# Performance work log

Measured on AMD Instinct MI355X. Metric: run time of the kernel, lower is better.

The kernel has to match this reference:

```python
import jax, jax.numpy as jnp
import numpy as np

LATENT = 128
RNN = 512      # rnn_size
CODE = 2048    # code_size


def _lstm_cell(x, h, c, w_ih, w_hh, b_ih, b_hh):
    # PyTorch LSTM gate order: i, f, g, o
    gates = x @ w_ih + b_ih + h @ w_hh + b_hh
    i, f, g, o = jnp.split(gates, 4, axis=-1)
    c_new = jax.nn.sigmoid(f) * c + jax.nn.sigmoid(i) * jnp.tanh(g)
    h_new = jax.nn.sigmoid(o) * jnp.tanh(c_new)
    return h_new, c_new


def setup_inputs() -> dict:
    key = jax.random.key(0)
    ks = jax.random.split(key, 16)
    B = 1024
    s = 0.02
    inp = {
        "latent": jax.random.normal(ks[0], (B, LATENT), jnp.float32),
        "num_segments": 128,
        # unpack_idea: Linear(latent, code) + Tanh
        "w_unpack": jax.random.normal(ks[1], (LATENT, CODE), jnp.float32) * s,
        "b_unpack": jnp.zeros((CODE,), jnp.float32),
        # LSTM layer 1 (input CODE -> hidden RNN)
        "w_ih1": jax.random.normal(ks[2], (CODE, 4 * RNN), jnp.float32) * s,
        "w_hh1": jax.random.normal(ks[3], (RNN, 4 * RNN), jnp.float32) * s,
        "b_ih1": jnp.zeros((4 * RNN,), jnp.float32),
        "b_hh1": jnp.zeros((4 * RNN,), jnp.float32),
        # LSTM layer 2 (hidden RNN -> hidden RNN)
        "w_ih2": jax.random.normal(ks[4], (RNN, 4 * RNN), jnp.float32) * s,
        "w_hh2": jax.random.normal(ks[5], (RNN, 4 * RNN), jnp.float32) * s,
        "b_ih2": jnp.zeros((4 * RNN,), jnp.float32),
        "b_hh2": jnp.zeros((4 * RNN,), jnp.float32),
        # attention head: Linear(RNN, CODE) + Sigmoid
        "w_att": jax.random.normal(ks[6], (RNN, CODE), jnp.float32) * s,
        "b_att": jnp.zeros((CODE,), jnp.float32),
        # widths head: Linear(RNN, 1) + Sigmoid
        "w_wid": jax.random.normal(ks[7], (RNN, 1), jnp.float32) * s,
        "b_wid": jnp.zeros((1,), jnp.float32),
        # angles head: Linear(RNN, 1) + Tanh
        "w_ang": jax.random.normal(ks[8], (RNN, 1), jnp.float32) * s,
        "b_ang": jnp.zeros((1,), jnp.float32),
    }
    return inp


def reference(latent, num_segments, w_unpack, b_unpack,
              w_ih1, w_hh1, b_ih1, b_hh1,
              w_ih2, w_hh2, b_ih2, b_hh2,
              w_att, b_att, w_wid, b_wid, w_ang, b_ang):
    B = latent.shape[0]
    idea = jnp.tanh(latent @ w_unpack + b_unpack)  # [B, CODE]

    def step(carry, _):
        h1, c1, h2, c2, att = carry
        x = idea * att                               # gated input [B, CODE]
        h1, c1 = _lstm_cell(x, h1, c1, w_ih1, w_hh1, b_ih1, b_hh1)
        h2, c2 = _lstm_cell(h1, h2, c2, w_ih2, w_hh2, b_ih2, b_hh2)
        angles = jnp.tanh(h2 @ w_ang + b_ang)        # [B, 1]
        widths = jax.nn.sigmoid(h2 @ w_wid + b_wid)  # [B, 1]
        att = jax.nn.sigmoid(h2 @ w_att + b_att)     # [B, CODE]
        out = jnp.concatenate([angles, widths], axis=-1)  # [B, 2]
        return (h1, c1, h2, c2, att), out

    z = jnp.zeros((B, RNN), latent.dtype)
    init = (z, z, z, z, jnp.ones((B, CODE), latent.dtype))
    _, ys = jax.lax.scan(step, init, None, length=int(num_segments))
    return jnp.transpose(ys, (1, 0, 2))  # [B, num_segments, 2]
```

## Files before the change

### kernel.cpp

```cpp
#include <hip/hip_runtime.h>
#include <hip/hip_bf16.h>
#include <cmath>

typedef __attribute__((ext_vector_type(8))) short bf16x8;
typedef __attribute__((ext_vector_type(4))) float f32x4;
typedef unsigned int u32;

#define DEVI __device__ __forceinline__

DEVI float sigf(float x) { return 1.0f / (1.0f + __expf(-x)); }

typedef const __attribute__((address_space(1))) u32* gas_t;
typedef __attribute__((address_space(3))) u32* las_t;
DEVI void g2l16(const void* g, void* l) {
  __builtin_amdgcn_global_load_lds((gas_t)g, (las_t)l, 16, 0, 0);
}

#define BATCH 1024
#define CODE  2048
#define RNN   512
#define NG    2048
#define TSTEPS 128
#define K1K   2560
#define K2K   1024
#define K3K   512
#define NO    2176

#define BUFSZ 24576


__global__ void conv_w1(const float* __restrict__ w_ih1, const float* __restrict__ w_hh1,
                        __hip_bfloat16* __restrict__ W1T) {
  int np = blockIdx.x;
  int co = (np & 3) * RNN + (np >> 2);
  for (int k = threadIdx.x; k < K1K; k += 256) {
    float v = (k < CODE) ? w_ih1[(size_t)k * NG + co]
                         : w_hh1[(size_t)(k - CODE) * NG + co];
    W1T[(size_t)np * K1K + k] = __float2bfloat16(v);
  }
}

__global__ void conv_w2(const float* __restrict__ w_ih2, const float* __restrict__ w_hh2,
                        __hip_bfloat16* __restrict__ W2T) {
  int np = blockIdx.x;
  int co = (np & 3) * RNN + (np >> 2);
  for (int k = threadIdx.x; k < K2K; k += 256) {
    float v = (k < RNN) ? w_ih2[(size_t)k * NG + co]
                        : w_hh2[(size_t)(k - RNN) * NG + co];
    W2T[(size_t)np * K2K + k] = __float2bfloat16(v);
  }
}

__global__ void conv_wo(const float* __restrict__ w_att, const float* __restrict__ w_ang,
                        const float* __restrict__ w_wid, __hip_bfloat16* __restrict__ WoT) {
  int n = blockIdx.x;
  for (int k = threadIdx.x; k < K3K; k += 256) {
    float v = 0.f;
    if (n < CODE) v = w_att[(size_t)k * CODE + n];
    else if (n == CODE) v = w_ang[k];
    else if (n == CODE + 1) v = w_wid[k];
    WoT[(size_t)n * K3K + k] = __float2bfloat16(v);
  }
}

__global__ void conv_b(const float* b_ih1, const float* b_hh1,
                       const float* b_ih2, const float* b_hh2,
                       const float* b_att, const float* b_ang, const float* b_wid,
                       float* b1p, float* b2p, float* bo) {
  int i = blockIdx.x * 256 + threadIdx.x;
  if (i < NG) {
    int co = (i & 3) * RNN + (i >> 2);
    b1p[i] = b_ih1[co] + b_hh1[co];
    b2p[i] = b_ih2[co] + b_hh2[co];
  }
  if (i < NO) {
    float v = 0.f;
    if (i < CODE) v = b_att[i];
    else if (i == CODE) v = b_ang[0];
    else if (i == CODE + 1) v = b_wid[0];
    bo[i] = v;
  }
}

__global__ void init_zero(char* __restrict__ zb, char* __restrict__ xb) {
  int idx = blockIdx.x * 256 + threadIdx.x;
  f32x4 z = {0.f, 0.f, 0.f, 0.f};
  for (int i = idx; i < 393216; i += 262144) *(f32x4*)(zb + (size_t)i * 16) = z;
  for (int i = idx; i < 65536; i += 262144) {
    int row = i >> 6, j = i & 63;
    *(f32x4*)(xb + (size_t)row * (K1K * 2) + CODE * 2 + (size_t)j * 16) = z;
  }
}

__global__ void idea_kernel(const float* __restrict__ latent, const float* __restrict__ w,
                            const float* __restrict__ b,
                            __hip_bfloat16* __restrict__ idea_bf,
                            __hip_bfloat16* __restrict__ x_bf) {
  int idx = blockIdx.x * 256 + threadIdx.x;
  int bi = idx >> 11, j = idx & 2047;
  const float* lr = latent + bi * 128;
  float s = b[j];
#pragma unroll 8
  for (int k = 0; k < 128; ++k) s = fmaf(lr[k], w[(size_t)k * CODE + j], s);
  __hip_bfloat16 h = __float2bfloat16(tanhf(s));
  idea_bf[idx] = h;
  x_bf[(size_t)bi * K1K + j] = h;
}


#define STAGE(KO, DST)                                                        \
  _Pragma("unroll") for (int j = 0; j < 3; ++j)                               \
      g2l16(gp[j] + (KO), (DST) + ldsc[j]);

#define COMPUTE(SB)                                                           \
  __builtin_amdgcn_s_setprio(1);                                              \
  _Pragma("unroll") for (int kk = 0; kk < 2; ++kk) {                          \
    bf16x8 av[2], bv[2];                                                      \
    _Pragma("unroll") for (int fm = 0; fm < 2; ++fm)                          \
        av[fm] = *(const bf16x8*)((SB) + aoff[fm][kk]);                       \
    _Pragma("unroll") for (int fn = 0; fn < 2; ++fn)                          \
        bv[fn] = *(const bf16x8*)((SB) + boff[fn][kk]);                       \
    _Pragma("unroll") for (int fm = 0; fm < 2; ++fm)                          \
      _Pragma("unroll") for (int fn = 0; fn < 2; ++fn)                        \
        acc[fm][fn] = __builtin_amdgcn_mfma_f32_16x16x32_bf16(                \
            av[fm], bv[fn], acc[fm][fn], 0, 0, 0);                            \
  }                                                                           \
  __builtin_amdgcn_s_setprio(0);

#define WAITB(N)                                                              \
  asm volatile("s_waitcnt vmcnt(" #N ")" ::: "memory");                       \
  __builtin_amdgcn_s_barrier();                                               \
  asm volatile("" ::: "memory");

__global__ void __launch_bounds__(512, 2)
lstm_gemm(const char* __restrict__ Ab, const char* __restrict__ Bb,
          int K, int nk, const float* __restrict__ bias,
          float* __restrict__ c_state, __hip_bfloat16* __restrict__ h_out, int h_ld) {
  __shared__ char smem[3 * BUFSZ];
  const int tid = threadIdx.x;
  const int l = blockIdx.x;
  const int xcd = l & 7, bi = l >> 3;
  const int n0 = ((xcd << 1) | (bi & 1)) * 128;
  const int m0 = (bi >> 1) * 64;
  const int kb = K * 2;

  const int lane = tid & 63, wv = tid >> 6;
  const int rl = lane >> 3;
  const int cswz = ((lane & 7) * 16) ^ (rl << 4);

  const char* gp[3];
  int ldsc[3];
#pragma unroll
  for (int j = 0; j < 3; ++j) {
    int c = wv * 3 + j;
    int row = (c < 8) ? (m0 + c * 8 + rl) : (n0 + (c - 8) * 8 + rl);
    const char* base = (c < 8) ? Ab : Bb;
    gp[j] = base + (size_t)row * kb + cswz;
    ldsc[j] = c * 1024;
  }

  const int l16 = lane & 15, lg = lane >> 4;
  const int wr = wv & 1, wc = wv >> 1;
  const int xm = (l16 & 7) << 4;

  int aoff[2][2], boff[2][2];
#pragma unroll
  for (int fm = 0; fm < 2; ++fm) {
    int r = wr * 32 + fm * 16 + l16;
#pragma unroll
    for (int kk = 0; kk < 2; ++kk) aoff[fm][kk] = r * 128 + ((kk * 64 + lg * 16) ^ xm);
  }
#pragma unroll
  for (int fn = 0; fn < 2; ++fn) {
    int r = wc * 32 + fn * 16 + l16;
#pragma unroll
    for (int kk = 0; kk < 2; ++kk) boff[fn][kk] = 8192 + r * 128 + ((kk * 64 + lg * 16) ^ xm);
  }

  f32x4 z4 = {0.f, 0.f, 0.f, 0.f};
  f32x4 acc[2][2];
#pragma unroll
  for (int a = 0; a < 2; ++a)
#pragma unroll
    for (int b = 0; b < 2; ++b) acc[a][b] = z4;

  STAGE(0, smem);
  STAGE(128, smem + BUFSZ);

  for (int kt = 0; kt < nk - 1; ++kt) {
    WAITB(3);
    if (kt + 2 < nk) {
      char* nb = smem + ((kt + 2) % 3) * BUFSZ;
      STAGE((size_t)(kt + 2) * 128, nb);
    }
    const char* sb = smem + (kt % 3) * BUFSZ;
    COMPUTE(sb);
  }
  WAITB(0);
  COMPUTE(smem + ((nk - 1) % 3) * BUFSZ);

  __syncthreads();
  float* gsm = (float*)smem;
#pragma unroll
  for (int fm = 0; fm < 2; ++fm)
#pragma unroll
    for (int fn = 0; fn < 2; ++fn) {
      int col = wc * 32 + fn * 16 + l16;
#pragma unroll
      for (int j = 0; j < 4; ++j) {
        int row = wr * 32 + fm * 16 + lg * 4 + j;
        gsm[row * 128 + col] = acc[fm][fn][j];
      }
    }
  __syncthreads();
#pragma unroll
  for (int i = 0; i < 4; ++i) {
    int p = tid + i * 512;
    int unit = p & 31, row = p >> 5;
    f32x4 g = *(const f32x4*)(gsm + row * 128 + unit * 4);
    f32x4 bb = *(const f32x4*)(bias + n0 + unit * 4);
    float ig = sigf(g.x + bb.x);
    float fg = sigf(g.y + bb.y);
    float gg = tanhf(g.z + bb.z);
    float og = sigf(g.w + bb.w);
    int grow = m0 + row, gu = (n0 >> 2) + unit;
    float cold = c_state[grow * RNN + gu];
    float cn = fg * cold + ig * gg;
    c_state[grow * RNN + gu] = cn;
    h_out[(size_t)grow * h_ld + gu] = __float2bfloat16(og * tanhf(cn));
  }
}

__global__ void __launch_bounds__(512, 2)
att_head(const char* __restrict__ Ab, const char* __restrict__ Bb,
         const float* __restrict__ bo,
         const __hip_bfloat16* __restrict__ idea_bf,
         __hip_bfloat16* __restrict__ x_bf,
         __hip_bfloat16* __restrict__ h_cat,
         const __hip_bfloat16* __restrict__ h2b,
         float* __restrict__ out, int t) {
  __shared__ char smem[3 * BUFSZ];
  const int tid = threadIdx.x;
  const int m0 = blockIdx.x * 64;
  const int n0 = blockIdx.y * 128;
  const int kb = K3K * 2;

  if (blockIdx.y == 0) {
#pragma unroll
    for (int i = 0; i < 8; ++i) {
      int o = tid * 16 + i * 8192;
      int row = m0 + (o >> 10), cb = o & 1023;
      *(f32x4*)((char*)x_bf + (size_t)row * (K1K * 2) + CODE * 2 + cb) =
          *(const f32x4*)((const char*)h_cat + (size_t)row * (K2K * 2) + cb);
      *(f32x4*)((char*)h_cat + (size_t)row * (K2K * 2) + RNN * 2 + cb) =
          *(const f32x4*)((const char*)h2b + (size_t)row * (RNN * 2) + cb);
    }
  }

  const int lane = tid & 63, wv = tid >> 6;
  const int rl = lane >> 3;
  const int cswz = ((lane & 7) * 16) ^ (rl << 4);

  const char* gp[3];
  int ldsc[3];
#pragma unroll
  for (int j = 0; j < 3; ++j) {
    int c = wv * 3 + j;
    int row = (c < 8) ? (m0 + c * 8 + rl) : (n0 + (c - 8) * 8 + rl);
    const char* base = (c < 8) ? Ab : Bb;
    gp[j] = base + (size_t)row * kb + cswz;
    ldsc[j] = c * 1024;
  }

  const int l16 = lane & 15, lg = lane >> 4;
  const int wr = wv & 1, wc = wv >> 1;
  const int xm = (l16 & 7) << 4;

  int aoff[2][2], boff[2][2];
#pragma unroll
  for (int fm = 0; fm < 2; ++fm) {
    int r = wr * 32 + fm * 16 + l16;
#pragma unroll
    for (int kk = 0; kk < 2; ++kk) aoff[fm][kk] = r * 128 + ((kk * 64 + lg * 16) ^ xm);
  }
#pragma unroll
  for (int fn = 0; fn < 2; ++fn) {
    int r = wc * 32 + fn * 16 + l16;
#pragma unroll
    for (int kk = 0; kk < 2; ++kk) boff[fn][kk] = 8192 + r * 128 + ((kk * 64 + lg * 16) ^ xm);
  }

  f32x4 z4 = {0.f, 0.f, 0.f, 0.f};
  f32x4 acc[2][2];
#pragma unroll
  for (int a = 0; a < 2; ++a)
#pragma unroll
    for (int b = 0; b < 2; ++b) acc[a][b] = z4;

  const int nk = K3K / 64;
  STAGE(0, smem);
  STAGE(128, smem + BUFSZ);

  for (int kt = 0; kt < nk - 1; ++kt) {
    WAITB(3);
    if (kt + 2 < nk) {
      char* nb = smem + ((kt + 2) % 3) * BUFSZ;
      STAGE((size_t)(kt + 2) * 128, nb);
    }
    const char* sb = smem + (kt % 3) * BUFSZ;
    COMPUTE(sb);
  }
  WAITB(0);
  COMPUTE(smem + ((nk - 1) % 3) * BUFSZ);

#pragma unroll
  for (int fn = 0; fn < 2; ++fn) {
    int col = n0 + wc * 32 + fn * 16 + l16;
    float bia = bo[col];
    bool is_att = col < CODE;
#pragma unroll
    for (int fm = 0; fm < 2; ++fm)
#pragma unroll
      for (int j = 0; j < 4; ++j) {
        int row = m0 + wr * 32 + fm * 16 + lg * 4 + j;
        float v = acc[fm][fn][j] + bia;
        if (is_att) {
          float a = sigf(v);
          float id = __bfloat162float(idea_bf[(size_t)row * CODE + col]);
          x_bf[(size_t)row * K1K + col] = __float2bfloat16(id * a);
        } else if (col == CODE) {
          out[row * (TSTEPS * 2) + t * 2] = tanhf(v);
        } else if (col == CODE + 1) {
          out[row * (TSTEPS * 2) + t * 2 + 1] = sigf(v);
        }
      }
  }
}

extern "C" void kernel_launch(void* const* d_in, const int* in_sizes, int n_in,
                              void* d_out, int out_size, void* d_ws, size_t ws_size,
                              hipStream_t stream) {
  const float* latent = (const float*)d_in[0];
  const float* w_unp  = (const float*)d_in[2];
  const float* b_unp  = (const float*)d_in[3];
  const float* w_ih1  = (const float*)d_in[4];
  const float* w_hh1  = (const float*)d_in[5];
  const float* b_ih1  = (const float*)d_in[6];
  const float* b_hh1  = (const float*)d_in[7];
  const float* w_ih2  = (const float*)d_in[8];
  const float* w_hh2  = (const float*)d_in[9];
  const float* b_ih2  = (const float*)d_in[10];
  const float* b_hh2  = (const float*)d_in[11];
  const float* w_att  = (const float*)d_in[12];
  const float* b_att  = (const float*)d_in[13];
  const float* w_wid  = (const float*)d_in[14];
  const float* b_wid  = (const float*)d_in[15];
  const float* w_ang  = (const float*)d_in[16];
  const float* b_ang  = (const float*)d_in[17];
  float* out = (float*)d_out;

  char* ws = (char*)d_ws;
  __hip_bfloat16* W1T  = (__hip_bfloat16*)(ws + 0);
  __hip_bfloat16* W2T  = (__hip_bfloat16*)(ws + 10485760);
  __hip_bfloat16* WoT  = (__hip_bfloat16*)(ws + 14680064);
  float* b1p           = (float*)(ws + 16908288);
  float* b2p           = (float*)(ws + 16916480);
  float* bo            = (float*)(ws + 16924672);
  __hip_bfloat16* idea = (__hip_bfloat16*)(ws + 16933376);
  __hip_bfloat16* x_bf = (__hip_bfloat16*)(ws + 21127680);
  __hip_bfloat16* hcat = (__hip_bfloat16*)(ws + 26370560);
  float* c1            = (float*)(ws + 28467712);
  float* c2            = (float*)(ws + 30564864);
  __hip_bfloat16* h2b  = (__hip_bfloat16*)(ws + 32662016);

  conv_w1<<<2048, 256, 0, stream>>>(w_ih1, w_hh1, W1T);
  conv_w2<<<2048, 256, 0, stream>>>(w_ih2, w_hh2, W2T);
  conv_wo<<<2176, 256, 0, stream>>>(w_att, w_ang, w_wid, WoT);
  conv_b<<<9, 256, 0, stream>>>(b_ih1, b_hh1, b_ih2, b_hh2, b_att, b_ang, b_wid, b1p, b2p, bo);
  init_zero<<<1024, 256, 0, stream>>>(ws + 26370560, (char*)x_bf);
  idea_kernel<<<8192, 256, 0, stream>>>(latent, w_unp, b_unp, idea, x_bf);

  for (int t = 0; t < TSTEPS; ++t) {
    lstm_gemm<<<256, 512, 0, stream>>>((const char*)x_bf, (const char*)W1T,
                                       K1K, K1K / 64, b1p, c1, hcat, 1024);
    lstm_gemm<<<256, 512, 0, stream>>>((const char*)hcat, (const char*)W2T,
                                       K2K, K2K / 64, b2p, c2, h2b, 512);
    att_head<<<dim3(16, 17), 512, 0, stream>>>((const char*)h2b, (const char*)WoT,
                                               bo, idea, x_bf, hcat, h2b, out, t);
  }
}
```

Measured before the change: 5.710 ms.

## Split K across wave halves with 128-wide K tiles and LDS reduction

The GEMM kernels now stage 128-wide K tiles (doubled LDS buffers) and split the eight waves into two K-halves. Each wave computes a 32x64 sub-tile over half of each K tile. The two halves are then summed through padded shared memory before the LSTM and attention epilogues. The goal is fewer pipeline iterations and barriers, and more MFMA work per LDS load. In exchange it uses more LDS (144KB per block), which may lower occupancy below two blocks per CU, and it adds a reduction pass.

```diff
diff --git a/kernel.cpp b/kernel.cpp
--- a/kernel.cpp
+++ b/kernel.cpp
@@ -26,7 +26,7 @@
 #define K3K   512
 #define NO    2176
 
-#define BUFSZ 24576
+#define BUFSZ 49152
 
 
 __global__ void conv_w1(const float* __restrict__ w_ih1, const float* __restrict__ w_hh1,
@@ -109,19 +109,19 @@
 
 
 #define STAGE(KO, DST)                                                        \
-  _Pragma("unroll") for (int j = 0; j < 3; ++j)                               \
+  _Pragma("unroll") for (int j = 0; j < 6; ++j)                               \
       g2l16(gp[j] + (KO), (DST) + ldsc[j]);
 
 #define COMPUTE(SB)                                                           \
   __builtin_amdgcn_s_setprio(1);                                              \
   _Pragma("unroll") for (int kk = 0; kk < 2; ++kk) {                          \
-    bf16x8 av[2], bv[2];                                                      \
+    bf16x8 av[2], bv[4];                                                      \
     _Pragma("unroll") for (int fm = 0; fm < 2; ++fm)                          \
         av[fm] = *(const bf16x8*)((SB) + aoff[fm][kk]);                       \
-    _Pragma("unroll") for (int fn = 0; fn < 2; ++fn)                          \
+    _Pragma("unroll") for (int fn = 0; fn < 4; ++fn)                          \
         bv[fn] = *(const bf16x8*)((SB) + boff[fn][kk]);                       \
     _Pragma("unroll") for (int fm = 0; fm < 2; ++fm)                          \
-      _Pragma("unroll") for (int fn = 0; fn < 2; ++fn)                        \
+      _Pragma("unroll") for (int fn = 0; fn < 4; ++fn)                        \
         acc[fm][fn] = __builtin_amdgcn_mfma_f32_16x16x32_bf16(                \
             av[fm], bv[fn], acc[fm][fn], 0, 0, 0);                            \
   }                                                                           \
@@ -131,6 +131,74 @@
   asm volatile("s_waitcnt vmcnt(" #N ")" ::: "memory");                       \
   __builtin_amdgcn_s_barrier();                                               \
   asm volatile("" ::: "memory");
+
+#define GEMM_SETUP(AB, BB, KBYTES)                                            \
+  const int lane = tid & 63, wv = tid >> 6;                                   \
+  const char* gp[6]; int ldsc[6];                                             \
+  {                                                                           \
+    int ccol = ((lane & 15) * 16) ^ ((lane >> 4) << 4);                       \
+    _Pragma("unroll") for (int j = 0; j < 6; ++j) {                           \
+      int c = wv * 6 + j;                                                     \
+      int row = (c < 16) ? (m0 + c * 4 + (lane >> 4))                         \
+                         : (n0 + (c - 16) * 4 + (lane >> 4));                 \
+      const char* base = (c < 16) ? (AB) : (BB);                              \
+      gp[j] = base + (size_t)row * (KBYTES) + (ccol ^ ((c & 1) << 6));        \
+      ldsc[j] = c * 1024;                                                     \
+    }                                                                         \
+  }                                                                           \
+  const int l16 = lane & 15, lg = lane >> 4;                                  \
+  const int kh = wv >> 2, q = wv & 3, wr = q & 1, wc = q >> 1;                \
+  const int xm = (l16 & 7) << 4;                                              \
+  int aoff[2][2], boff[4][2];                                                 \
+  _Pragma("unroll") for (int fm = 0; fm < 2; ++fm) {                          \
+    int r = wr * 32 + fm * 16 + l16;                                          \
+    _Pragma("unroll") for (int kk = 0; kk < 2; ++kk)                          \
+      aoff[fm][kk] = r * 256 + ((kh * 128 + kk * 64 + lg * 16) ^ xm);         \
+  }                                                                           \
+  _Pragma("unroll") for (int fn = 0; fn < 4; ++fn) {                          \
+    int r = wc * 64 + fn * 16 + l16;                                          \
+    _Pragma("unroll") for (int kk = 0; kk < 2; ++kk)                          \
+      boff[fn][kk] = 16384 + r * 256 + ((kh * 128 + kk * 64 + lg * 16) ^ xm); \
+  }                                                                           \
+  f32x4 z4 = {0.f, 0.f, 0.f, 0.f};                                            \
+  f32x4 acc[2][4];                                                            \
+  _Pragma("unroll") for (int a = 0; a < 2; ++a)                               \
+    _Pragma("unroll") for (int b = 0; b < 4; ++b) acc[a][b] = z4;
+
+#define GEMM_PIPELINE(NK)                                                     \
+  STAGE(0, smem);                                                             \
+  STAGE(256, smem + BUFSZ);                                                   \
+  for (int kt = 0; kt < (NK) - 1; ++kt) {                                     \
+    WAITB(6);                                                                 \
+    if (kt + 2 < (NK)) {                                                      \
+      char* nb = smem + ((kt + 2) % 3) * BUFSZ;                               \
+      STAGE((size_t)(kt + 2) * 256, nb);                                      \
+    }                                                                         \
+    const char* sb = smem + (kt % 3) * BUFSZ;                                 \
+    COMPUTE(sb);                                                              \
+  }                                                                           \
+  WAITB(0);                                                                   \
+  COMPUTE(smem + (((NK) - 1) % 3) * BUFSZ);
+
+#define KH_COMBINE()                                                          \
+  __syncthreads();                                                            \
+  float* gsm = (float*)smem;                                                  \
+  if (kh == 1) {                                                              \
+    _Pragma("unroll") for (int fm = 0; fm < 2; ++fm)                          \
+      _Pragma("unroll") for (int fn = 0; fn < 4; ++fn)                        \
+        _Pragma("unroll") for (int j = 0; j < 4; ++j)                         \
+          gsm[(wr * 32 + fm * 16 + lg * 4 + j) * 132 +                        \
+              wc * 64 + fn * 16 + l16] = acc[fm][fn][j];                      \
+  }                                                                           \
+  __syncthreads();                                                            \
+  if (kh == 0) {                                                              \
+    _Pragma("unroll") for (int fm = 0; fm < 2; ++fm)                          \
+      _Pragma("unroll") for (int fn = 0; fn < 4; ++fn)                        \
+        _Pragma("unroll") for (int j = 0; j < 4; ++j)                         \
+          gsm[(wr * 32 + fm * 16 + lg * 4 + j) * 132 +                        \
+              wc * 64 + fn * 16 + l16] += acc[fm][fn][j];                     \
+  }                                                                           \
+  __syncthreads();
 
 __global__ void __launch_bounds__(512, 2)
 lstm_gemm(const char* __restrict__ Ab, const char* __restrict__ Bb,
@@ -144,80 +212,15 @@
   const int m0 = (bi >> 1) * 64;
   const int kb = K * 2;
 
-  const int lane = tid & 63, wv = tid >> 6;
-  const int rl = lane >> 3;
-  const int cswz = ((lane & 7) * 16) ^ (rl << 4);
-
-  const char* gp[3];
-  int ldsc[3];
-#pragma unroll
-  for (int j = 0; j < 3; ++j) {
-    int c = wv * 3 + j;
-    int row = (c < 8) ? (m0 + c * 8 + rl) : (n0 + (c - 8) * 8 + rl);
-    const char* base = (c < 8) ? Ab : Bb;
-    gp[j] = base + (size_t)row * kb + cswz;
-    ldsc[j] = c * 1024;
-  }
-
-  const int l16 = lane & 15, lg = lane >> 4;
-  const int wr = wv & 1, wc = wv >> 1;
-  const int xm = (l16 & 7) << 4;
-
-  int aoff[2][2], boff[2][2];
-#pragma unroll
-  for (int fm = 0; fm < 2; ++fm) {
-    int r = wr * 32 + fm * 16 + l16;
-#pragma unroll
-    for (int kk = 0; kk < 2; ++kk) aoff[fm][kk] = r * 128 + ((kk * 64 + lg * 16) ^ xm);
-  }
-#pragma unroll
-  for (int fn = 0; fn < 2; ++fn) {
-    int r = wc * 32 + fn * 16 + l16;
-#pragma unroll
-    for (int kk = 0; kk < 2; ++kk) boff[fn][kk] = 8192 + r * 128 + ((kk * 64 + lg * 16) ^ xm);
-  }
-
-  f32x4 z4 = {0.f, 0.f, 0.f, 0.f};
-  f32x4 acc[2][2];
-#pragma unroll
-  for (int a = 0; a < 2; ++a)
-#pragma unroll
-    for (int b = 0; b < 2; ++b) acc[a][b] = z4;
-
-  STAGE(0, smem);
-  STAGE(128, smem + BUFSZ);
-
-  for (int kt = 0; kt < nk - 1; ++kt) {
-    WAITB(3);
-    if (kt + 2 < nk) {
-      char* nb = smem + ((kt + 2) % 3) * BUFSZ;
-      STAGE((size_t)(kt + 2) * 128, nb);
-    }
-    const char* sb = smem + (kt % 3) * BUFSZ;
-    COMPUTE(sb);
-  }
-  WAITB(0);
-  COMPUTE(smem + ((nk - 1) % 3) * BUFSZ);
-
-  __syncthreads();
-  float* gsm = (float*)smem;
-#pragma unroll
-  for (int fm = 0; fm < 2; ++fm)
-#pragma unroll
-    for (int fn = 0; fn < 2; ++fn) {
-      int col = wc * 32 + fn * 16 + l16;
-#pragma unroll
-      for (int j = 0; j < 4; ++j) {
-        int row = wr * 32 + fm * 16 + lg * 4 + j;
-        gsm[row * 128 + col] = acc[fm][fn][j];
-      }
-    }
-  __syncthreads();
+  GEMM_SETUP(Ab, Bb, kb)
+  GEMM_PIPELINE(nk)
+  KH_COMBINE()
+
 #pragma unroll
   for (int i = 0; i < 4; ++i) {
     int p = tid + i * 512;
     int unit = p & 31, row = p >> 5;
-    f32x4 g = *(const f32x4*)(gsm + row * 128 + unit * 4);
+    f32x4 g = *(const f32x4*)(gsm + row * 132 + unit * 4);
     f32x4 bb = *(const f32x4*)(bias + n0 + unit * 4);
     float ig = sigf(g.x + bb.x);
     float fg = sigf(g.y + bb.y);
@@ -257,83 +260,27 @@
     }
   }
 
-  const int lane = tid & 63, wv = tid >> 6;
-  const int rl = lane >> 3;
-  const int cswz = ((lane & 7) * 16) ^ (rl << 4);
-
-  const char* gp[3];
-  int ldsc[3];
+  GEMM_SETUP(Ab, Bb, kb)
+  const int nk = K3K / 128;
+  GEMM_PIPELINE(nk)
+  KH_COMBINE()
+
 #pragma unroll
-  for (int j = 0; j < 3; ++j) {
-    int c = wv * 3 + j;
-    int row = (c < 8) ? (m0 + c * 8 + rl) : (n0 + (c - 8) * 8 + rl);
-    const char* base = (c < 8) ? Ab : Bb;
-    gp[j] = base + (size_t)row * kb + cswz;
-    ldsc[j] = c * 1024;
-  }
-
-  const int l16 = lane & 15, lg = lane >> 4;
-  const int wr = wv & 1, wc = wv >> 1;
-  const int xm = (l16 & 7) << 4;
-
-  int aoff[2][2], boff[2][2];
-#pragma unroll
-  for (int fm = 0; fm < 2; ++fm) {
-    int r = wr * 32 + fm * 16 + l16;
-#pragma unroll
-    for (int kk = 0; kk < 2; ++kk) aoff[fm][kk] = r * 128 + ((kk * 64 + lg * 16) ^ xm);
-  }
-#pragma unroll
-  for (int fn = 0; fn < 2; ++fn) {
-    int r = wc * 32 + fn * 16 + l16;
-#pragma unroll
-    for (int kk = 0; kk < 2; ++kk) boff[fn][kk] = 8192 + r * 128 + ((kk * 64 + lg * 16) ^ xm);
-  }
-
-  f32x4 z4 = {0.f, 0.f, 0.f, 0.f};
-  f32x4 acc[2][2];
-#pragma unroll
-  for (int a = 0; a < 2; ++a)
-#pragma unroll
-    for (int b = 0; b < 2; ++b) acc[a][b] = z4;
-
-  const int nk = K3K / 64;
-  STAGE(0, smem);
-  STAGE(128, smem + BUFSZ);
-
-  for (int kt = 0; kt < nk - 1; ++kt) {
-    WAITB(3);
-    if (kt + 2 < nk) {
-      char* nb = smem + ((kt + 2) % 3) * BUFSZ;
-      STAGE((size_t)(kt + 2) * 128, nb);
+  for (int i = 0; i < 16; ++i) {
+    int p = tid + i * 512;
+    int cl = p & 127, row = p >> 7;
+    int col = n0 + cl;
+    float v = gsm[row * 132 + cl] + bo[col];
+    int grow = m0 + row;
+    if (col < CODE) {
+      float a = sigf(v);
+      float id = __bfloat162float(idea_bf[(size_t)grow * CODE + col]);
+      x_bf[(size_t)grow * K1K + col] = __float2bfloat16(id * a);
+    } else if (col == CODE) {
+      out[grow * (TSTEPS * 2) + t * 2] = tanhf(v);
+    } else if (col == CODE + 1) {
+      out[grow * (TSTEPS * 2) + t * 2 + 1] = sigf(v);
     }
-    const char* sb = smem + (kt % 3) * BUFSZ;
-    COMPUTE(sb);
-  }
-  WAITB(0);
-  COMPUTE(smem + ((nk - 1) % 3) * BUFSZ);
-
-#pragma unroll
-  for (int fn = 0; fn < 2; ++fn) {
-    int col = n0 + wc * 32 + fn * 16 + l16;
-    float bia = bo[col];
-    bool is_att = col < CODE;
-#pragma unroll
-    for (int fm = 0; fm < 2; ++fm)
-#pragma unroll
-      for (int j = 0; j < 4; ++j) {
-        int row = m0 + wr * 32 + fm * 16 + lg * 4 + j;
-        float v = acc[fm][fn][j] + bia;
-        if (is_att) {
-          float a = sigf(v);
-          float id = __bfloat162float(idea_bf[(size_t)row * CODE + col]);
-          x_bf[(size_t)row * K1K + col] = __float2bfloat16(id * a);
-        } else if (col == CODE) {
-          out[row * (TSTEPS * 2) + t * 2] = tanhf(v);
-        } else if (col == CODE + 1) {
-          out[row * (TSTEPS * 2) + t * 2 + 1] = sigf(v);
-        }
-      }
   }
 }
 
@@ -382,9 +329,9 @@
 
   for (int t = 0; t < TSTEPS; ++t) {
     lstm_gemm<<<256, 512, 0, stream>>>((const char*)x_bf, (const char*)W1T,
-                                       K1K, K1K / 64, b1p, c1, hcat, 1024);
+                                       K1K, K1K / 128, b1p, c1, hcat, 1024);
     lstm_gemm<<<256, 512, 0, stream>>>((const char*)hcat, (const char*)W2T,
-                                       K2K, K2K / 64, b2p, c2, h2b, 512);
+                                       K2K, K2K / 128, b2p, c2, h2b, 512);
     att_head<<<dim3(16, 17), 512, 0, stream>>>((const char*)h2b, (const char*)WoT,
                                                bo, idea, x_bf, hcat, h2b, out, t);
   }
```

Result: slower. 6.810 ms (+19.3%).
